# Optimization experiments

Hardware: AMD Instinct MI355X
Metric: run time of the kernel (lower is better)

## Reference

```python
import jax, jax.numpy as jnp
import numpy as np

CUTOFF = 8.0
NUM_G = 50
HID = 128
NUM_INTER = 3
NUM_NODES = 50000
NUM_EDGES = 1600000
NUM_GRAPHS = 128
MAX_Z = 100
LOG2 = float(np.log(2.0))


def ssp(x):
    # PyG ShiftedSoftplus
    return jax.nn.softplus(x) - LOG2


def setup_inputs() -> dict:
    key = jax.random.key(0)
    ks = jax.random.split(key, 20)
    s = 0.1
    pos = jax.random.normal(ks[0], (NUM_NODES, 3), dtype=jnp.float32) * 4.0
    edge_shift = jax.random.normal(ks[1], (NUM_EDGES, 3), dtype=jnp.float32) * 0.5
    z = jax.random.randint(ks[2], (NUM_NODES,), 0, MAX_Z, dtype=jnp.int32)
    edge_index = jax.random.randint(ks[3], (2, NUM_EDGES), 0, NUM_NODES, dtype=jnp.int32)
    batch = jnp.sort(jax.random.randint(ks[4], (NUM_NODES,), 0, NUM_GRAPHS, dtype=jnp.int32))
    emb = jax.random.normal(ks[5], (MAX_Z, HID), dtype=jnp.float32) * s
    mlp_w1 = jax.random.normal(ks[6], (NUM_INTER, NUM_G, HID), dtype=jnp.float32) * s
    mlp_b1 = jnp.zeros((NUM_INTER, HID), jnp.float32)
    mlp_w2 = jax.random.normal(ks[7], (NUM_INTER, HID, HID), dtype=jnp.float32) * s
    mlp_b2 = jnp.zeros((NUM_INTER, HID), jnp.float32)
    cf_w1 = jax.random.normal(ks[8], (NUM_INTER, HID, HID), dtype=jnp.float32) * s  # no bias (PyG lin1)
    cf_w2 = jax.random.normal(ks[9], (NUM_INTER, HID, HID), dtype=jnp.float32) * s
    cf_b2 = jnp.zeros((NUM_INTER, HID), jnp.float32)
    lin_w = jax.random.normal(ks[10], (NUM_INTER, HID, HID), dtype=jnp.float32) * s
    lin_b = jnp.zeros((NUM_INTER, HID), jnp.float32)
    head_w1 = jax.random.normal(ks[11], (HID, HID // 2), dtype=jnp.float32) * s
    head_b1 = jnp.zeros((HID // 2,), jnp.float32)
    head_w2 = jax.random.normal(ks[12], (HID // 2, 1), dtype=jnp.float32) * s
    head_b2 = jnp.zeros((1,), jnp.float32)
    return dict(pos=pos, edge_shift=edge_shift, emb=emb, mlp_w1=mlp_w1, mlp_b1=mlp_b1,
                mlp_w2=mlp_w2, mlp_b2=mlp_b2, cf_w1=cf_w1, cf_w2=cf_w2, cf_b2=cf_b2,
                lin_w=lin_w, lin_b=lin_b, head_w1=head_w1, head_b1=head_b1,
                head_w2=head_w2, head_b2=head_b2, z=z, edge_index=edge_index, batch=batch)


def reference(pos, edge_shift, emb, mlp_w1, mlp_b1, mlp_w2, mlp_b2, cf_w1, cf_w2, cf_b2,
              lin_w, lin_b, head_w1, head_b1, head_w2, head_b2, z, edge_index, batch):
    src, dst = edge_index[0], edge_index[1]
    # edge distances: pos[row] - (pos[col] + shift)
    rel = pos[src] - (pos[dst] + edge_shift)            # [E,3]
    w = jnp.linalg.norm(rel, axis=-1)                   # [E]
    # Gaussian smearing
    offset = jnp.linspace(0.0, CUTOFF, NUM_G, dtype=pos.dtype)
    coeff = -0.5 / (offset[1] - offset[0]) ** 2
    edge_attr = jnp.exp(coeff * (w[:, None] - offset) ** 2)   # [E,50]
    # cosine cutoff
    C = 0.5 * (jnp.cos(w * jnp.pi / CUTOFF) + 1.0)            # [E]
    h = emb[z]                                                # [N,128]
    for i in range(NUM_INTER):
        Wf = (ssp(edge_attr @ mlp_w1[i] + mlp_b1[i]) @ mlp_w2[i] + mlp_b2[i]) * C[:, None]  # [E,128]
        msg = (h @ cf_w1[i])[src] * Wf                   # gather-multiply  [E,128]
        agg = jax.ops.segment_sum(msg, dst, num_segments=NUM_NODES)         # scatter-sum [N,128]
        h = h + (ssp(agg @ cf_w2[i] + cf_b2[i]) @ lin_w[i] + lin_b[i])
    out_atom = ssp(h @ head_w1 + head_b1) @ head_w2 + head_b2               # [N,1]
    sums = jax.ops.segment_sum(out_atom, batch, num_segments=NUM_GRAPHS)    # [G,1]
    counts = jax.ops.segment_sum(jnp.ones((NUM_NODES, 1), out_atom.dtype), batch, num_segments=NUM_GRAPHS)
    return sums / jnp.maximum(counts, 1.0)  # mean readout; out_proj is Identity (128==128)
```

## Files before the change

kernel.cpp:

```cpp
#include <hip/hip_runtime.h>
#include <math.h>

#define NNODES  50000
#define NEDGES  1600000
#define NGRAPHS 128
#define HID     128
#define NG      50
#define NITER   3
#define TPTS    2048
#define WMAX    12.0f
#define PI_F    3.14159265358979323846f

__device__ __forceinline__ float ssp(float x) {
    float sp = fmaxf(x, 0.0f) + log1pf(expf(-fabsf(x)));
    return sp - 0.69314718055994530942f;
}

__global__ __launch_bounds__(256) void k_init_h(const float* __restrict__ emb,
                                                const int* __restrict__ z,
                                                float* __restrict__ h)
{
    int idx = blockIdx.x * 256 + threadIdx.x;
    int n = idx >> 7, c = idx & 127;
    h[idx] = emb[(z[n] << 7) + c];
}

__global__ __launch_bounds__(128) void k_table(const float* __restrict__ W1,
                                               const float* __restrict__ B1,
                                               const float* __restrict__ W2,
                                               const float* __restrict__ B2,
                                               float* __restrict__ table)
{
    int it = blockIdx.x / TPTS;
    int pt = blockIdx.x - it * TPTS;
    const float* W1i = W1 + (size_t)it * NG * HID;
    const float* B1i = B1 + (size_t)it * HID;
    const float* W2i = W2 + (size_t)it * HID * HID;
    const float* B2i = B2 + (size_t)it * HID;

    float w = pt * (WMAX / (float)(TPTS - 1));
    __shared__ float sEA[NG];
    __shared__ float sT1[HID];
    int k = threadIdx.x;
    if (k < NG) {
        float dx = 8.0f / 49.0f;
        float coeff = -0.5f / (dx * dx);
        float diff = w - (float)k * dx;
        sEA[k] = expf(coeff * diff * diff);
    }
    __syncthreads();
    float acc = B1i[k];
    for (int g = 0; g < NG; ++g) acc = fmaf(sEA[g], W1i[g * HID + k], acc);
    sT1[k] = ssp(acc);
    __syncthreads();
    float acc2 = B2i[k];
    for (int j = 0; j < HID; ++j) acc2 = fmaf(sT1[j], W2i[j * HID + k], acc2);
    table[(size_t)blockIdx.x * HID + k] = acc2;
}

__global__ __launch_bounds__(256) void k_tdelta(const float* __restrict__ raw,
                                                float* __restrict__ ti)
{
    int idx = blockIdx.x * 256 + threadIdx.x;
    int c = idx & 127;
    int pt_it = idx >> 7;
    int pt = pt_it & (TPTS - 1);
    float v = raw[idx];
    float nv = (pt == TPTS - 1) ? v : raw[idx + HID];
    ti[(size_t)pt_it * 256 + c * 2]     = v;
    ti[(size_t)pt_it * 256 + c * 2 + 1] = nv - v;
}

__global__ __launch_bounds__(256) void k_hist(const int* __restrict__ ei,
                                              int* __restrict__ deg)
{
    int e = blockIdx.x * 256 + threadIdx.x;
    if (e >= NEDGES) return;
    atomicAdd(&deg[ei[NEDGES + e]], 1);
}

#define SCAN_T 1024
#define CHUNK  49
__global__ __launch_bounds__(SCAN_T) void k_scan(const int* __restrict__ deg,
                                                 int* __restrict__ rowptr,
                                                 int* __restrict__ cursor)
{
    int tid = threadIdx.x;
    int base = tid * CHUNK;
    int vals[CHUNK];
    int local = 0;
    #pragma unroll
    for (int i = 0; i < CHUNK; ++i) {
        int idx = base + i;
        int v = (idx < NNODES) ? deg[idx] : 0;
        vals[i] = local;
        local += v;
    }
    int lane = tid & 63, wid = tid >> 6;
    int x = local;
    #pragma unroll
    for (int off = 1; off < 64; off <<= 1) {
        int y = __shfl_up(x, off);
        if (lane >= off) x += y;
    }
    __shared__ int wsum[16];
    __shared__ int woff[17];
    if (lane == 63) wsum[wid] = x;
    __syncthreads();
    if (tid == 0) {
        int acc = 0;
        #pragma unroll
        for (int i = 0; i < 16; ++i) { woff[i] = acc; acc += wsum[i]; }
        woff[16] = acc;
    }
    __syncthreads();
    int threadExcl = woff[wid] + x - local;
    #pragma unroll
    for (int i = 0; i < CHUNK; ++i) {
        int idx = base + i;
        if (idx < NNODES) {
            int p = threadExcl + vals[i];
            rowptr[idx] = p;
            cursor[idx] = p;
        }
    }
    if (tid == SCAN_T - 1) rowptr[NNODES] = woff[16];
}

__global__ __launch_bounds__(256) void k_scatter(const int* __restrict__ ei,
                                                 const float* __restrict__ pos,
                                                 const float* __restrict__ shift,
                                                 int* __restrict__ cursor,
                                                 float2* __restrict__ rec)
{
    int e = blockIdx.x * 256 + threadIdx.x;
    if (e >= NEDGES) return;
    int s = ei[e], d = ei[NEDGES + e];
    float rx = pos[3*s+0] - (pos[3*d+0] + shift[3*e+0]);
    float ry = pos[3*s+1] - (pos[3*d+1] + shift[3*e+1]);
    float rz = pos[3*s+2] - (pos[3*d+2] + shift[3*e+2]);
    float w = sqrtf(rx*rx + ry*ry + rz*rz);
    int slot = atomicAdd(&cursor[d], 1);
    rec[slot] = make_float2(__int_as_float(s), w);
}

__global__ __launch_bounds__(256) void k_gather(const float2* __restrict__ rec,
                                                const int* __restrict__ rowptr,
                                                const float* __restrict__ hf,
                                                const float* __restrict__ tableI,
                                                float* __restrict__ agg)
{
    int node = blockIdx.x * 4 + (threadIdx.x >> 6);
    int lane = threadIdx.x & 63;
    int beg = rowptr[node], end = rowptr[node + 1];
    const float SCALE = (float)(TPTS - 1) / WMAX;
    float2 acc = make_float2(0.f, 0.f);
    int k = beg;
    for (; k + 2 <= end; k += 2) {
        float2 r0 = rec[k];
        float2 r1 = rec[k + 1];
        int   s0 = __float_as_int(r0.x);
        int   s1 = __float_as_int(r1.x);
        float w0 = r0.y, w1 = r1.y;
        float t0 = fminf(w0 * SCALE, (float)(TPTS - 1));
        float t1 = fminf(w1 * SCALE, (float)(TPTS - 1));
        int i0 = (int)t0; if (i0 > TPTS - 2) i0 = TPTS - 2;
        int i1 = (int)t1; if (i1 > TPTS - 2) i1 = TPTS - 2;
        float fr0 = t0 - (float)i0;
        float fr1 = t1 - (float)i1;
        float4 ta = *((const float4*)(tableI + (size_t)i0 * 256) + lane);
        float4 tb = *((const float4*)(tableI + (size_t)i1 * 256) + lane);
        float2 h0 = *(const float2*)(hf + (size_t)s0 * HID + lane * 2);
        float2 h1 = *(const float2*)(hf + (size_t)s1 * HID + lane * 2);
        float C0 = 0.5f * (__cosf(w0 * (PI_F / 8.0f)) + 1.0f);
        float C1 = 0.5f * (__cosf(w1 * (PI_F / 8.0f)) + 1.0f);
        float f0a = fmaf(fr0, ta.y, ta.x) * C0;
        float f0b = fmaf(fr0, ta.w, ta.z) * C0;
        float f1a = fmaf(fr1, tb.y, tb.x) * C1;
        float f1b = fmaf(fr1, tb.w, tb.z) * C1;
        acc.x = fmaf(f0a, h0.x, acc.x);
        acc.y = fmaf(f0b, h0.y, acc.y);
        acc.x = fmaf(f1a, h1.x, acc.x);
        acc.y = fmaf(f1b, h1.y, acc.y);
    }
    if (k < end) {
        float2 r0 = rec[k];
        int   s0 = __float_as_int(r0.x);
        float w0 = r0.y;
        float t0 = fminf(w0 * SCALE, (float)(TPTS - 1));
        int i0 = (int)t0; if (i0 > TPTS - 2) i0 = TPTS - 2;
        float fr0 = t0 - (float)i0;
        float4 ta = *((const float4*)(tableI + (size_t)i0 * 256) + lane);
        float2 h0 = *(const float2*)(hf + (size_t)s0 * HID + lane * 2);
        float C0 = 0.5f * (__cosf(w0 * (PI_F / 8.0f)) + 1.0f);
        float f0a = fmaf(fr0, ta.y, ta.x) * C0;
        float f0b = fmaf(fr0, ta.w, ta.z) * C0;
        acc.x = fmaf(f0a, h0.x, acc.x);
        acc.y = fmaf(f0b, h0.y, acc.y);
    }
    *(float2*)(agg + (size_t)node * HID + lane * 2) = acc;
}

__global__ __launch_bounds__(256) void k_node_gemm(const float* __restrict__ A,
                                                   const float* __restrict__ W,
                                                   const float* __restrict__ bias,
                                                   float* __restrict__ out)
{
    __shared__ float sA[64 * 132];
    int r0 = blockIdx.x * 64;
    int tid = threadIdx.x;
    for (int idx = tid; idx < 64 * 32; idx += 256) {
        int r = idx >> 5, c4 = idx & 31;
        int row = r0 + r;
        float4 v = make_float4(0.f, 0.f, 0.f, 0.f);
        if (row < NNODES) v = *(const float4*)(A + (size_t)row * HID + c4 * 4);
        *(float4*)(&sA[r * 132 + c4 * 4]) = v;
    }
    __syncthreads();
    int tx = tid & 15, ty = tid >> 4;
    int cc = tx * 8, ee = ty * 4;
    float acc[4][8];
    if (bias) {
        float4 b0 = *(const float4*)(bias + cc);
        float4 b1 = *(const float4*)(bias + cc + 4);
        #pragma unroll
        for (int e = 0; e < 4; ++e) {
            acc[e][0]=b0.x; acc[e][1]=b0.y; acc[e][2]=b0.z; acc[e][3]=b0.w;
            acc[e][4]=b1.x; acc[e][5]=b1.y; acc[e][6]=b1.z; acc[e][7]=b1.w;
        }
    } else {
        #pragma unroll
        for (int e = 0; e < 4; ++e)
            #pragma unroll
            for (int c = 0; c < 8; ++c) acc[e][c] = 0.f;
    }
    for (int j = 0; j < HID; ++j) {
        float a[4];
        #pragma unroll
        for (int e = 0; e < 4; ++e) a[e] = sA[(ee + e) * 132 + j];
        float4 w0 = *(const float4*)(W + (size_t)j * HID + cc);
        float4 w1 = *(const float4*)(W + (size_t)j * HID + cc + 4);
        float wv[8] = {w0.x,w0.y,w0.z,w0.w,w1.x,w1.y,w1.z,w1.w};
        #pragma unroll
        for (int e = 0; e < 4; ++e)
            #pragma unroll
            for (int c = 0; c < 8; ++c)
                acc[e][c] = fmaf(a[e], wv[c], acc[e][c]);
    }
    #pragma unroll
    for (int e = 0; e < 4; ++e) {
        int row = r0 + ee + e;
        if (row < NNODES) {
            *(float4*)(out + (size_t)row * HID + cc)     = make_float4(acc[e][0], acc[e][1], acc[e][2], acc[e][3]);
            *(float4*)(out + (size_t)row * HID + cc + 4) = make_float4(acc[e][4], acc[e][5], acc[e][6], acc[e][7]);
        }
    }
}

__global__ __launch_bounds__(256) void k_node_update(const float* __restrict__ agg,
                                                     const float* __restrict__ W,
                                                     const float* __restrict__ B,
                                                     const float* __restrict__ L,
                                                     const float* __restrict__ LB,
                                                     float* __restrict__ h)
{
    __shared__ float sA[64 * 132];
    __shared__ float sT[64 * 132];
    int r0 = blockIdx.x * 64;
    int tid = threadIdx.x;
    for (int idx = tid; idx < 64 * 32; idx += 256) {
        int r = idx >> 5, c4 = idx & 31;
        int row = r0 + r;
        float4 v = make_float4(0.f, 0.f, 0.f, 0.f);
        if (row < NNODES) v = *(const float4*)(agg + (size_t)row * HID + c4 * 4);
        *(float4*)(&sA[r * 132 + c4 * 4]) = v;
    }
    __syncthreads();
    int tx = tid & 15, ty = tid >> 4;
    int cc = tx * 8, ee = ty * 4;
    float acc[4][8];
    {
        float4 b0 = *(const float4*)(B + cc);
        float4 b1 = *(const float4*)(B + cc + 4);
        #pragma unroll
        for (int e = 0; e < 4; ++e) {
            acc[e][0]=b0.x; acc[e][1]=b0.y; acc[e][2]=b0.z; acc[e][3]=b0.w;
            acc[e][4]=b1.x; acc[e][5]=b1.y; acc[e][6]=b1.z; acc[e][7]=b1.w;
        }
    }
    for (int j = 0; j < HID; ++j) {
        float a[4];
        #pragma unroll
        for (int e = 0; e < 4; ++e) a[e] = sA[(ee + e) * 132 + j];
        float4 w0 = *(const float4*)(W + (size_t)j * HID + cc);
        float4 w1 = *(const float4*)(W + (size_t)j * HID + cc + 4);
        float wv[8] = {w0.x,w0.y,w0.z,w0.w,w1.x,w1.y,w1.z,w1.w};
        #pragma unroll
        for (int e = 0; e < 4; ++e)
            #pragma unroll
            for (int c = 0; c < 8; ++c)
                acc[e][c] = fmaf(a[e], wv[c], acc[e][c]);
    }
    #pragma unroll
    for (int e = 0; e < 4; ++e)
        #pragma unroll
        for (int c = 0; c < 8; ++c)
            sT[(ee + e) * 132 + cc + c] = ssp(acc[e][c]);
    __syncthreads();
    float acc2[4][8];
    {
        float4 b0 = *(const float4*)(LB + cc);
        float4 b1 = *(const float4*)(LB + cc + 4);
        #pragma unroll
        for (int e = 0; e < 4; ++e) {
            acc2[e][0]=b0.x; acc2[e][1]=b0.y; acc2[e][2]=b0.z; acc2[e][3]=b0.w;
            acc2[e][4]=b1.x; acc2[e][5]=b1.y; acc2[e][6]=b1.z; acc2[e][7]=b1.w;
        }
    }
    for (int j = 0; j < HID; ++j) {
        float a[4];
        #pragma unroll
        for (int e = 0; e < 4; ++e) a[e] = sT[(ee + e) * 132 + j];
        float4 w0 = *(const float4*)(L + (size_t)j * HID + cc);
        float4 w1 = *(const float4*)(L + (size_t)j * HID + cc + 4);
        float wv[8] = {w0.x,w0.y,w0.z,w0.w,w1.x,w1.y,w1.z,w1.w};
        #pragma unroll
        for (int e = 0; e < 4; ++e)
            #pragma unroll
            for (int c = 0; c < 8; ++c)
                acc2[e][c] = fmaf(a[e], wv[c], acc2[e][c]);
    }
    #pragma unroll
    for (int e = 0; e < 4; ++e) {
        int row = r0 + ee + e;
        if (row < NNODES) {
            float4* hp0 = (float4*)(h + (size_t)row * HID + cc);
            float4* hp1 = (float4*)(h + (size_t)row * HID + cc + 4);
            float4 h0 = *hp0, h1 = *hp1;
            h0.x += acc2[e][0]; h0.y += acc2[e][1]; h0.z += acc2[e][2]; h0.w += acc2[e][3];
            h1.x += acc2[e][4]; h1.y += acc2[e][5]; h1.z += acc2[e][6]; h1.w += acc2[e][7];
            *hp0 = h0; *hp1 = h1;
        }
    }
}

__global__ __launch_bounds__(256) void k_head(const float* __restrict__ h,
                                              const float* __restrict__ w1,
                                              const float* __restrict__ b1,
                                              const float* __restrict__ w2,
                                              const float* __restrict__ b2,
                                              const int* __restrict__ batch,
                                              float* __restrict__ sums_pad)
{
    __shared__ float sA[64 * 132];
    int r0 = blockIdx.x * 64;
    int tid = threadIdx.x;
    for (int idx = tid; idx < 64 * 32; idx += 256) {
        int r = idx >> 5, c4 = idx & 31;
        int row = r0 + r;
        float4 v = make_float4(0.f, 0.f, 0.f, 0.f);
        if (row < NNODES) v = *(const float4*)(h + (size_t)row * HID + c4 * 4);
        *(float4*)(&sA[r * 132 + c4 * 4]) = v;
    }
    __syncthreads();
    int tx = tid & 7, ty = tid >> 3;
    int cc = tx * 8, ee = ty * 2;
    float acc[2][8];
    {
        float4 b0 = *(const float4*)(b1 + cc);
        float4 bb = *(const float4*)(b1 + cc + 4);
        #pragma unroll
        for (int e = 0; e < 2; ++e) {
            acc[e][0]=b0.x; acc[e][1]=b0.y; acc[e][2]=b0.z; acc[e][3]=b0.w;
            acc[e][4]=bb.x; acc[e][5]=bb.y; acc[e][6]=bb.z; acc[e][7]=bb.w;
        }
    }
    #pragma unroll 4
    for (int j = 0; j < HID; ++j) {
        float a0 = sA[(ee + 0) * 132 + j];
        float a1 = sA[(ee + 1) * 132 + j];
        float4 w0 = *(const float4*)(w1 + (size_t)j * 64 + cc);
        float4 wv1 = *(const float4*)(w1 + (size_t)j * 64 + cc + 4);
        float wv[8] = {w0.x,w0.y,w0.z,w0.w,wv1.x,wv1.y,wv1.z,wv1.w};
        #pragma unroll
        for (int c = 0; c < 8; ++c) {
            acc[0][c] = fmaf(a0, wv[c], acc[0][c]);
            acc[1][c] = fmaf(a1, wv[c], acc[1][c]);
        }
    }
    float4 w2a = *(const float4*)(w2 + cc);
    float4 w2b = *(const float4*)(w2 + cc + 4);
    float w2v[8] = {w2a.x,w2a.y,w2a.z,w2a.w,w2b.x,w2b.y,w2b.z,w2b.w};
    float bias2 = b2[0];
    #pragma unroll
    for (int e = 0; e < 2; ++e) {
        float part = 0.f;
        #pragma unroll
        for (int c = 0; c < 8; ++c) part = fmaf(ssp(acc[e][c]), w2v[c], part);
        part += __shfl_down(part, 4, 8);
        part += __shfl_down(part, 2, 8);
        part += __shfl_down(part, 1, 8);
        if (tx == 0) {
            int row = r0 + ee + e;
            if (row < NNODES) {
                int b = batch[row];
                atomicAdd(&sums_pad[b * 16], part + bias2);
            }
        }
    }
}

__global__ void k_final(const float* __restrict__ sums_pad,
                        const int* __restrict__ batch,
                        float* __restrict__ out)
{
    int g = threadIdx.x;
    if (g >= NGRAPHS) return;
    int lo = 0, hi = NNODES;
    while (lo < hi) { int mid = (lo + hi) >> 1; if (batch[mid] < g) lo = mid + 1; else hi = mid; }
    int a = lo;
    lo = 0; hi = NNODES;
    while (lo < hi) { int mid = (lo + hi) >> 1; if (batch[mid] < g + 1) lo = mid + 1; else hi = mid; }
    float cnt = (float)(lo - a);
    out[g] = sums_pad[g * 16] / fmaxf(cnt, 1.0f);
}

extern "C" void kernel_launch(void* const* d_in, const int* in_sizes, int n_in,
                              void* d_out, int out_size, void* d_ws, size_t ws_size,
                              hipStream_t stream)
{
    const float* pos     = (const float*)d_in[0];
    const float* shift   = (const float*)d_in[1];
    const float* emb     = (const float*)d_in[2];
    const float* mlp_w1  = (const float*)d_in[3];
    const float* mlp_b1  = (const float*)d_in[4];
    const float* mlp_w2  = (const float*)d_in[5];
    const float* mlp_b2  = (const float*)d_in[6];
    const float* cf_w1   = (const float*)d_in[7];
    const float* cf_w2   = (const float*)d_in[8];
    const float* cf_b2   = (const float*)d_in[9];
    const float* lin_w   = (const float*)d_in[10];
    const float* lin_b   = (const float*)d_in[11];
    const float* head_w1 = (const float*)d_in[12];
    const float* head_b1 = (const float*)d_in[13];
    const float* head_w2 = (const float*)d_in[14];
    const float* head_b2 = (const float*)d_in[15];
    const int*   z       = (const int*)d_in[16];
    const int*   ei      = (const int*)d_in[17];
    const int*   batch   = (const int*)d_in[18];
    float* out = (float*)d_out;

    float* ws = (float*)d_ws;
    size_t off = 0;
    float*  h       = ws + off; off += (size_t)NNODES * HID;
    float*  hf      = ws + off; off += (size_t)NNODES * HID;
    float*  agg     = ws + off; off += (size_t)NNODES * HID;
    float*  rawT    = ws + off; off += (size_t)3 * TPTS * HID;
    float*  tableI  = ws + off; off += (size_t)3 * TPTS * HID * 2;
    float2* rec     = (float2*)(ws + off); off += (size_t)2 * NEDGES;
    int*    rowptr  = (int*)(ws + off); off += NNODES + 1;
    int*    deg     = (int*)(ws + off); off += NNODES;
    int*    cursor  = (int*)(ws + off); off += NNODES;
    float*  sums_pad= ws + off; off += NGRAPHS * 16;

    hipMemsetAsync(deg, 0, NNODES * sizeof(int), stream);
    hipMemsetAsync(sums_pad, 0, NGRAPHS * 16 * sizeof(float), stream);

    k_hist<<<(NEDGES + 255) / 256, 256, 0, stream>>>(ei, deg);
    k_scan<<<1, SCAN_T, 0, stream>>>(deg, rowptr, cursor);
    k_scatter<<<(NEDGES + 255) / 256, 256, 0, stream>>>(ei, pos, shift, cursor, rec);

    k_init_h<<<NNODES * HID / 256, 256, 0, stream>>>(emb, z, h);
    k_table<<<3 * TPTS, 128, 0, stream>>>(mlp_w1, mlp_b1, mlp_w2, mlp_b2, rawT);
    k_tdelta<<<(3 * TPTS * HID) / 256, 256, 0, stream>>>(rawT, tableI);

    for (int i = 0; i < NITER; ++i) {
        k_node_gemm<<<(NNODES + 63) / 64, 256, 0, stream>>>(h, cf_w1 + (size_t)i * HID * HID, nullptr, hf);
        k_gather<<<NNODES / 4, 256, 0, stream>>>(rec, rowptr, hf, tableI + (size_t)i * TPTS * HID * 2, agg);
        k_node_update<<<(NNODES + 63) / 64, 256, 0, stream>>>(agg, cf_w2 + (size_t)i * HID * HID,
                                                              cf_b2 + (size_t)i * HID,
                                                              lin_w + (size_t)i * HID * HID,
                                                              lin_b + (size_t)i * HID, h);
    }
    k_head<<<(NNODES + 63) / 64, 256, 0, stream>>>(h, head_w1, head_b1, head_w2, head_b2, batch, sums_pad);
    k_final<<<1, 128, 0, stream>>>(sums_pad, batch, out);
}
```

Measured before the change: 1.227 ms.

## Store filter table and gathered node features in fp16, enlarge node GEMM tiles

Converts the interpolation table and the per-iteration transformed node features (hf) to half precision, which halves the bytes moved by the bandwidth-bound edge gather. The gather loop is unrolled to four edges with two accumulator pairs to expose more memory-level parallelism. The node GEMM, update and head kernels move to 128-row tiles with 512 threads, and the update kernel reuses one shared buffer instead of two. The trade-off is reduced precision in the message values and higher shared-memory use per block.

```diff
diff --git a/kernel.cpp b/kernel.cpp
--- a/kernel.cpp
+++ b/kernel.cpp
@@ -1,4 +1,5 @@
 #include <hip/hip_runtime.h>
+#include <hip/hip_fp16.h>
 #include <math.h>
 
 #define NNODES  50000
@@ -59,7 +60,7 @@
 }
 
 __global__ __launch_bounds__(256) void k_tdelta(const float* __restrict__ raw,
-                                                float* __restrict__ ti)
+                                                __half* __restrict__ ti)
 {
     int idx = blockIdx.x * 256 + threadIdx.x;
     int c = idx & 127;
@@ -67,8 +68,8 @@
     int pt = pt_it & (TPTS - 1);
     float v = raw[idx];
     float nv = (pt == TPTS - 1) ? v : raw[idx + HID];
-    ti[(size_t)pt_it * 256 + c * 2]     = v;
-    ti[(size_t)pt_it * 256 + c * 2 + 1] = nv - v;
+    ti[(size_t)pt_it * 256 + c * 2]     = __float2half(v);
+    ti[(size_t)pt_it * 256 + c * 2 + 1] = __float2half(nv - v);
 }
 
 __global__ __launch_bounds__(256) void k_hist(const int* __restrict__ ei,
@@ -144,72 +145,63 @@
     rec[slot] = make_float2(__int_as_float(s), w);
 }
 
+__device__ __forceinline__ void edge_contrib(float2 r, int lane,
+                                             const __half2* __restrict__ hfH,
+                                             const __half* __restrict__ tableH,
+                                             float& ax, float& ay)
+{
+    int   s = __float_as_int(r.x);
+    float w = r.y;
+    const float SCALE = (float)(TPTS - 1) / WMAX;
+    float t = fminf(w * SCALE, (float)(TPTS - 1));
+    int i0 = (int)t; if (i0 > TPTS - 2) i0 = TPTS - 2;
+    float fr = t - (float)i0;
+    float C = 0.5f * (__cosf(w * (PI_F / 8.0f)) + 1.0f);
+    uint2 tv = *((const uint2*)(tableH + (size_t)i0 * 256) + lane);
+    __half2 hv = hfH[(size_t)s * 64 + lane];
+    float2 p0 = __half22float2(*(__half2*)&tv.x);
+    float2 p1 = __half22float2(*(__half2*)&tv.y);
+    float2 hf2 = __half22float2(hv);
+    ax = fmaf(fmaf(fr, p0.y, p0.x) * C, hf2.x, ax);
+    ay = fmaf(fmaf(fr, p1.y, p1.x) * C, hf2.y, ay);
+}
+
 __global__ __launch_bounds__(256) void k_gather(const float2* __restrict__ rec,
                                                 const int* __restrict__ rowptr,
-                                                const float* __restrict__ hf,
-                                                const float* __restrict__ tableI,
+                                                const __half2* __restrict__ hfH,
+                                                const __half* __restrict__ tableH,
                                                 float* __restrict__ agg)
 {
     int node = blockIdx.x * 4 + (threadIdx.x >> 6);
     int lane = threadIdx.x & 63;
     int beg = rowptr[node], end = rowptr[node + 1];
-    const float SCALE = (float)(TPTS - 1) / WMAX;
-    float2 acc = make_float2(0.f, 0.f);
+    float ax0 = 0.f, ay0 = 0.f, ax1 = 0.f, ay1 = 0.f;
     int k = beg;
-    for (; k + 2 <= end; k += 2) {
+    for (; k + 4 <= end; k += 4) {
         float2 r0 = rec[k];
         float2 r1 = rec[k + 1];
-        int   s0 = __float_as_int(r0.x);
-        int   s1 = __float_as_int(r1.x);
-        float w0 = r0.y, w1 = r1.y;
-        float t0 = fminf(w0 * SCALE, (float)(TPTS - 1));
-        float t1 = fminf(w1 * SCALE, (float)(TPTS - 1));
-        int i0 = (int)t0; if (i0 > TPTS - 2) i0 = TPTS - 2;
-        int i1 = (int)t1; if (i1 > TPTS - 2) i1 = TPTS - 2;
-        float fr0 = t0 - (float)i0;
-        float fr1 = t1 - (float)i1;
-        float4 ta = *((const float4*)(tableI + (size_t)i0 * 256) + lane);
-        float4 tb = *((const float4*)(tableI + (size_t)i1 * 256) + lane);
-        float2 h0 = *(const float2*)(hf + (size_t)s0 * HID + lane * 2);
-        float2 h1 = *(const float2*)(hf + (size_t)s1 * HID + lane * 2);
-        float C0 = 0.5f * (__cosf(w0 * (PI_F / 8.0f)) + 1.0f);
-        float C1 = 0.5f * (__cosf(w1 * (PI_F / 8.0f)) + 1.0f);
-        float f0a = fmaf(fr0, ta.y, ta.x) * C0;
-        float f0b = fmaf(fr0, ta.w, ta.z) * C0;
-        float f1a = fmaf(fr1, tb.y, tb.x) * C1;
-        float f1b = fmaf(fr1, tb.w, tb.z) * C1;
-        acc.x = fmaf(f0a, h0.x, acc.x);
-        acc.y = fmaf(f0b, h0.y, acc.y);
-        acc.x = fmaf(f1a, h1.x, acc.x);
-        acc.y = fmaf(f1b, h1.y, acc.y);
-    }
-    if (k < end) {
+        float2 r2 = rec[k + 2];
+        float2 r3 = rec[k + 3];
+        edge_contrib(r0, lane, hfH, tableH, ax0, ay0);
+        edge_contrib(r1, lane, hfH, tableH, ax1, ay1);
+        edge_contrib(r2, lane, hfH, tableH, ax0, ay0);
+        edge_contrib(r3, lane, hfH, tableH, ax1, ay1);
+    }
+    for (; k < end; ++k) {
         float2 r0 = rec[k];
-        int   s0 = __float_as_int(r0.x);
-        float w0 = r0.y;
-        float t0 = fminf(w0 * SCALE, (float)(TPTS - 1));
-        int i0 = (int)t0; if (i0 > TPTS - 2) i0 = TPTS - 2;
-        float fr0 = t0 - (float)i0;
-        float4 ta = *((const float4*)(tableI + (size_t)i0 * 256) + lane);
-        float2 h0 = *(const float2*)(hf + (size_t)s0 * HID + lane * 2);
-        float C0 = 0.5f * (__cosf(w0 * (PI_F / 8.0f)) + 1.0f);
-        float f0a = fmaf(fr0, ta.y, ta.x) * C0;
-        float f0b = fmaf(fr0, ta.w, ta.z) * C0;
-        acc.x = fmaf(f0a, h0.x, acc.x);
-        acc.y = fmaf(f0b, h0.y, acc.y);
-    }
-    *(float2*)(agg + (size_t)node * HID + lane * 2) = acc;
-}
-
-__global__ __launch_bounds__(256) void k_node_gemm(const float* __restrict__ A,
+        edge_contrib(r0, lane, hfH, tableH, ax0, ay0);
+    }
+    *(float2*)(agg + (size_t)node * HID + lane * 2) = make_float2(ax0 + ax1, ay0 + ay1);
+}
+
+__global__ __launch_bounds__(512) void k_node_gemm(const float* __restrict__ A,
                                                    const float* __restrict__ W,
-                                                   const float* __restrict__ bias,
-                                                   float* __restrict__ out)
-{
-    __shared__ float sA[64 * 132];
-    int r0 = blockIdx.x * 64;
+                                                   __half* __restrict__ outH)
+{
+    __shared__ float sA[128 * 132];
+    int r0 = blockIdx.x * 128;
     int tid = threadIdx.x;
-    for (int idx = tid; idx < 64 * 32; idx += 256) {
+    for (int idx = tid; idx < 128 * 32; idx += 512) {
         int r = idx >> 5, c4 = idx & 31;
         int row = r0 + r;
         float4 v = make_float4(0.f, 0.f, 0.f, 0.f);
@@ -220,20 +212,10 @@
     int tx = tid & 15, ty = tid >> 4;
     int cc = tx * 8, ee = ty * 4;
     float acc[4][8];
-    if (bias) {
-        float4 b0 = *(const float4*)(bias + cc);
-        float4 b1 = *(const float4*)(bias + cc + 4);
-        #pragma unroll
-        for (int e = 0; e < 4; ++e) {
-            acc[e][0]=b0.x; acc[e][1]=b0.y; acc[e][2]=b0.z; acc[e][3]=b0.w;
-            acc[e][4]=b1.x; acc[e][5]=b1.y; acc[e][6]=b1.z; acc[e][7]=b1.w;
-        }
-    } else {
-        #pragma unroll
-        for (int e = 0; e < 4; ++e)
-            #pragma unroll
-            for (int c = 0; c < 8; ++c) acc[e][c] = 0.f;
-    }
+    #pragma unroll
+    for (int e = 0; e < 4; ++e)
+        #pragma unroll
+        for (int c = 0; c < 8; ++c) acc[e][c] = 0.f;
     for (int j = 0; j < HID; ++j) {
         float a[4];
         #pragma unroll
@@ -251,24 +233,29 @@
     for (int e = 0; e < 4; ++e) {
         int row = r0 + ee + e;
         if (row < NNODES) {
-            *(float4*)(out + (size_t)row * HID + cc)     = make_float4(acc[e][0], acc[e][1], acc[e][2], acc[e][3]);
-            *(float4*)(out + (size_t)row * HID + cc + 4) = make_float4(acc[e][4], acc[e][5], acc[e][6], acc[e][7]);
-        }
-    }
-}
-
-__global__ __launch_bounds__(256) void k_node_update(const float* __restrict__ agg,
+            __half2 p0 = __floats2half2_rn(acc[e][0], acc[e][1]);
+            __half2 p1 = __floats2half2_rn(acc[e][2], acc[e][3]);
+            __half2 p2 = __floats2half2_rn(acc[e][4], acc[e][5]);
+            __half2 p3 = __floats2half2_rn(acc[e][6], acc[e][7]);
+            uint4 pk;
+            pk.x = *(unsigned*)&p0; pk.y = *(unsigned*)&p1;
+            pk.z = *(unsigned*)&p2; pk.w = *(unsigned*)&p3;
+            *(uint4*)(outH + (size_t)row * HID + cc) = pk;
+        }
+    }
+}
+
+__global__ __launch_bounds__(512) void k_node_update(const float* __restrict__ agg,
                                                      const float* __restrict__ W,
                                                      const float* __restrict__ B,
                                                      const float* __restrict__ L,
                                                      const float* __restrict__ LB,
                                                      float* __restrict__ h)
 {
-    __shared__ float sA[64 * 132];
-    __shared__ float sT[64 * 132];
-    int r0 = blockIdx.x * 64;
+    __shared__ float sA[128 * 132];
+    int r0 = blockIdx.x * 128;
     int tid = threadIdx.x;
-    for (int idx = tid; idx < 64 * 32; idx += 256) {
+    for (int idx = tid; idx < 128 * 32; idx += 512) {
         int r = idx >> 5, c4 = idx & 31;
         int row = r0 + r;
         float4 v = make_float4(0.f, 0.f, 0.f, 0.f);
@@ -301,11 +288,12 @@
             for (int c = 0; c < 8; ++c)
                 acc[e][c] = fmaf(a[e], wv[c], acc[e][c]);
     }
+    __syncthreads();
     #pragma unroll
     for (int e = 0; e < 4; ++e)
         #pragma unroll
         for (int c = 0; c < 8; ++c)
-            sT[(ee + e) * 132 + cc + c] = ssp(acc[e][c]);
+            sA[(ee + e) * 132 + cc + c] = ssp(acc[e][c]);
     __syncthreads();
     float acc2[4][8];
     {
@@ -320,7 +308,7 @@
     for (int j = 0; j < HID; ++j) {
         float a[4];
         #pragma unroll
-        for (int e = 0; e < 4; ++e) a[e] = sT[(ee + e) * 132 + j];
+        for (int e = 0; e < 4; ++e) a[e] = sA[(ee + e) * 132 + j];
         float4 w0 = *(const float4*)(L + (size_t)j * HID + cc);
         float4 w1 = *(const float4*)(L + (size_t)j * HID + cc + 4);
         float wv[8] = {w0.x,w0.y,w0.z,w0.w,w1.x,w1.y,w1.z,w1.w};
@@ -344,7 +332,7 @@
     }
 }
 
-__global__ __launch_bounds__(256) void k_head(const float* __restrict__ h,
+__global__ __launch_bounds__(512) void k_head(const float* __restrict__ h,
                                               const float* __restrict__ w1,
                                               const float* __restrict__ b1,
                                               const float* __restrict__ w2,
@@ -352,10 +340,10 @@
                                               const int* __restrict__ batch,
                                               float* __restrict__ sums_pad)
 {
-    __shared__ float sA[64 * 132];
-    int r0 = blockIdx.x * 64;
+    __shared__ float sA[128 * 132];
+    int r0 = blockIdx.x * 128;
     int tid = threadIdx.x;
-    for (int idx = tid; idx < 64 * 32; idx += 256) {
+    for (int idx = tid; idx < 128 * 32; idx += 512) {
         int r = idx >> 5, c4 = idx & 31;
         int row = r0 + r;
         float4 v = make_float4(0.f, 0.f, 0.f, 0.f);
@@ -453,10 +441,10 @@
     float* ws = (float*)d_ws;
     size_t off = 0;
     float*  h       = ws + off; off += (size_t)NNODES * HID;
-    float*  hf      = ws + off; off += (size_t)NNODES * HID;
+    __half* hfH     = (__half*)(ws + off); off += (size_t)(NNODES + 48) * HID / 2;
     float*  agg     = ws + off; off += (size_t)NNODES * HID;
     float*  rawT    = ws + off; off += (size_t)3 * TPTS * HID;
-    float*  tableI  = ws + off; off += (size_t)3 * TPTS * HID * 2;
+    __half* tableH  = (__half*)(ws + off); off += (size_t)3 * TPTS * HID;
     float2* rec     = (float2*)(ws + off); off += (size_t)2 * NEDGES;
     int*    rowptr  = (int*)(ws + off); off += NNODES + 1;
     int*    deg     = (int*)(ws + off); off += NNODES;
@@ -472,16 +460,18 @@
 
     k_init_h<<<NNODES * HID / 256, 256, 0, stream>>>(emb, z, h);
     k_table<<<3 * TPTS, 128, 0, stream>>>(mlp_w1, mlp_b1, mlp_w2, mlp_b2, rawT);
-    k_tdelta<<<(3 * TPTS * HID) / 256, 256, 0, stream>>>(rawT, tableI);
-
+    k_tdelta<<<(3 * TPTS * HID) / 256, 256, 0, stream>>>(rawT, tableH);
+
+    int gblk = (NNODES + 127) / 128;
     for (int i = 0; i < NITER; ++i) {
-        k_node_gemm<<<(NNODES + 63) / 64, 256, 0, stream>>>(h, cf_w1 + (size_t)i * HID * HID, nullptr, hf);
-        k_gather<<<NNODES / 4, 256, 0, stream>>>(rec, rowptr, hf, tableI + (size_t)i * TPTS * HID * 2, agg);
-        k_node_update<<<(NNODES + 63) / 64, 256, 0, stream>>>(agg, cf_w2 + (size_t)i * HID * HID,
-                                                              cf_b2 + (size_t)i * HID,
-                                                              lin_w + (size_t)i * HID * HID,
-                                                              lin_b + (size_t)i * HID, h);
-    }
-    k_head<<<(NNODES + 63) / 64, 256, 0, stream>>>(h, head_w1, head_b1, head_w2, head_b2, batch, sums_pad);
+        k_node_gemm<<<gblk, 512, 0, stream>>>(h, cf_w1 + (size_t)i * HID * HID, hfH);
+        k_gather<<<NNODES / 4, 256, 0, stream>>>(rec, rowptr, (const __half2*)hfH,
+                                                 tableH + (size_t)i * TPTS * HID * 2, agg);
+        k_node_update<<<gblk, 512, 0, stream>>>(agg, cf_w2 + (size_t)i * HID * HID,
+                                                cf_b2 + (size_t)i * HID,
+                                                lin_w + (size_t)i * HID * HID,
+                                                lin_b + (size_t)i * HID, h);
+    }
+    k_head<<<gblk, 512, 0, stream>>>(h, head_w1, head_b1, head_w2, head_b2, batch, sums_pad);
     k_final<<<1, 128, 0, stream>>>(sums_pad, batch, out);
 }
```

After: 1.077 ms. -12.2%, faster.
